# Performance work log

Measured on AMD Instinct MI355X. Metric: run time of the kernel, lower is better.

The kernel has to match this reference:

```python
import jax, jax.numpy as jnp
import numpy as np

LN_EPS = 1e-5

def setup_inputs() -> dict:
    key = jax.random.key(0)
    ks = jax.random.split(key, 8)
    B, N, C = 8, 16384, 256
    x = jax.random.normal(ks[0], (B, N, C), dtype=jnp.float32)
    time_decay = jax.random.normal(ks[1], (C,), dtype=jnp.float32) * 0.1
    s = 1.0 / np.sqrt(C)
    W_k = jax.random.normal(ks[2], (C, C), dtype=jnp.float32) * s
    W_v = jax.random.normal(ks[3], (C, C), dtype=jnp.float32) * s
    W_r = jax.random.normal(ks[4], (C, C), dtype=jnp.float32) * s
    W_o = jax.random.normal(ks[5], (C, C), dtype=jnp.float32) * s
    ln_w = jnp.ones((C,), dtype=jnp.float32)
    ln_b = jnp.zeros((C,), dtype=jnp.float32)
    return {"x": x, "time_decay": time_decay, "W_k": W_k, "W_v": W_v,
            "W_r": W_r, "W_o": W_o, "ln_w": ln_w, "ln_b": ln_b}

def _layernorm(x, w, b):
    mu = jnp.mean(x, axis=-1, keepdims=True)
    var = jnp.mean(jnp.square(x - mu), axis=-1, keepdims=True)
    return (x - mu) * jax.lax.rsqrt(var + LN_EPS) * w + b

def reference(x, time_decay, W_k, W_v, W_r, W_o, ln_w, ln_b):
    # x: (B, N, C)
    xn = _layernorm(x, ln_w, ln_b)
    k = jnp.einsum('bnc,dc->bnd', xn, W_k)
    v = jnp.einsum('bnc,dc->bnd', xn, W_v)
    r = jax.nn.sigmoid(jnp.einsum('bnc,dc->bnd', xn, W_r))
    decay = jnp.exp(-jax.nn.relu(time_decay))  # (C,)

    def step(state, k_t):
        state = state * decay + k_t  # (B, C)
        return state, state

    k_tm = jnp.swapaxes(k, 0, 1)  # (N, B, C) time-major for scan
    init = jnp.zeros(k.shape[::2], dtype=x.dtype)  # (B, C)
    _, states = jax.lax.scan(step, init, k_tm)
    states = jnp.swapaxes(states, 0, 1)  # (B, N, C)
    y = r * (states + v)
    y = jnp.einsum('bnc,dc->bnd', y, W_o)
    return y
```

## Files before the change

kernel.cpp:

```cpp
#include <hip/hip_runtime.h>
#include <hip/hip_bf16.h>
#include <stdint.h>


typedef __attribute__((ext_vector_type(8))) short short8;
typedef __attribute__((ext_vector_type(4))) float f32x4;

static __device__ __forceinline__ unsigned short f2bf(float f) {
  __hip_bfloat16 h = __float2bfloat16(f);
  return *reinterpret_cast<unsigned short*>(&h);
}
static __device__ __forceinline__ float bf2f(unsigned short u) {
  unsigned int v = ((unsigned int)u) << 16;
  float f;
  __builtin_memcpy(&f, &v, 4);
  return f;
}

__global__ void ln_kernel(const float* __restrict__ x,
                          const float* __restrict__ w,
                          const float* __restrict__ b,
                          unsigned short* __restrict__ xn) {
  const int wv = threadIdx.x >> 6;
  const int ln = threadIdx.x & 63;
  const size_t row = (size_t)blockIdx.x * 4 + wv;
  const float4 v = reinterpret_cast<const float4*>(x)[row * 64 + ln];
  float s  = v.x + v.y + v.z + v.w;
  float sq = v.x * v.x + v.y * v.y + v.z * v.z + v.w * v.w;
#pragma unroll
  for (int off = 32; off; off >>= 1) {
    s  += __shfl_xor(s, off, 64);
    sq += __shfl_xor(sq, off, 64);
  }
  const float mu  = s * (1.0f / 256.0f);
  const float var = sq * (1.0f / 256.0f) - mu * mu;
  const float rs  = rsqrtf(var + 1e-5f);
  const float4 w4 = reinterpret_cast<const float4*>(w)[ln];
  const float4 b4 = reinterpret_cast<const float4*>(b)[ln];
  ushort4 o;
  o.x = f2bf((v.x - mu) * rs * w4.x + b4.x);
  o.y = f2bf((v.y - mu) * rs * w4.y + b4.y);
  o.z = f2bf((v.z - mu) * rs * w4.z + b4.z);
  o.w = f2bf((v.w - mu) * rs * w4.w + b4.w);
  reinterpret_cast<ushort4*>(xn)[row * 64 + ln] = o;
}

__global__ void cvt_weights(const float* __restrict__ Wk,
                            const float* __restrict__ Wv,
                            const float* __restrict__ Wr,
                            const float* __restrict__ Wo,
                            unsigned short* __restrict__ Wkvr,
                            unsigned short* __restrict__ Wob) {
  const int idx = blockIdx.x * 256 + threadIdx.x;
  if (idx < 768 * 256) {
    const int r = idx >> 8;
    const int c = idx & 255;
    const float* src = (r < 256) ? Wk : ((r < 512) ? Wv : Wr);
    Wkvr[idx] = f2bf(src[(r & 255) * 256 + c]);
  } else {
    const int j = idx - 768 * 256;
    Wob[j] = f2bf(Wo[j]);
  }
}

template <int EPI, int NY>
__global__ void gemm_bt(const unsigned short* __restrict__ A,
                        const unsigned short* __restrict__ Bt,
                        unsigned short* __restrict__ kbuf,
                        unsigned short* __restrict__ vbuf,
                        unsigned short* __restrict__ rbuf,
                        float* __restrict__ outf) {
  constexpr int K = 256;
  __shared__ unsigned short Als[128][64];
  __shared__ unsigned short Bls[128][64];

  const int tid = threadIdx.x;
  const int wv = tid >> 6;
  const int ln = tid & 63;
  const int bid = blockIdx.x;
  const int bm0 = (bid / NY) * 128;
  const int bn0 = (bid % NY) * 128;
  const int lq = ln >> 4;
  const int lm = ln & 15;

  f32x4 acc[4][4];
#pragma unroll
  for (int i = 0; i < 4; ++i)
#pragma unroll
    for (int j = 0; j < 4; ++j) acc[i][j] = (f32x4){0.f, 0.f, 0.f, 0.f};

  const int m0w = (wv >> 1) * 64;
  const int n0w = (wv & 1) * 64;

  const int srow = ln >> 3;
  const int schunk = (ln & 7) ^ srow;

  for (int kk0 = 0; kk0 < K; kk0 += 64) {
#pragma unroll
    for (int i = 0; i < 4; ++i) {
      const int rr = wv * 32 + i * 8;
      const unsigned short* gA = A + (size_t)(bm0 + rr + srow) * K + kk0 + schunk * 8;
      __builtin_amdgcn_global_load_lds(
          (const __attribute__((address_space(1))) void*)gA,
          (__attribute__((address_space(3))) void*)&Als[rr][0], 16, 0, 0);
      const unsigned short* gB = Bt + (size_t)(bn0 + rr + srow) * K + kk0 + schunk * 8;
      __builtin_amdgcn_global_load_lds(
          (const __attribute__((address_space(1))) void*)gB,
          (__attribute__((address_space(3))) void*)&Bls[rr][0], 16, 0, 0);
    }
    __syncthreads();
#pragma unroll
    for (int kk = 0; kk < 64; kk += 32) {
      short8 af[4], bfr[4];
      const int chunk = (kk >> 3) + lq;
#pragma unroll
      for (int t = 0; t < 4; ++t) {
        const int rowa = m0w + t * 16 + lm;
        af[t] = *reinterpret_cast<const short8*>(&Als[rowa][(chunk ^ (rowa & 7)) * 8]);
        const int rowb = n0w + t * 16 + lm;
        bfr[t] = *reinterpret_cast<const short8*>(&Bls[rowb][(chunk ^ (rowb & 7)) * 8]);
      }
#pragma unroll
      for (int mt = 0; mt < 4; ++mt)
#pragma unroll
        for (int nt = 0; nt < 4; ++nt)
          acc[mt][nt] = __builtin_amdgcn_mfma_f32_16x16x32_bf16(
              bfr[nt], af[mt], acc[mt][nt], 0, 0, 0);
    }
    __syncthreads();
  }

#pragma unroll
  for (int mt = 0; mt < 4; ++mt) {
    const int m_g = bm0 + m0w + mt * 16 + lm;
#pragma unroll
    for (int nt = 0; nt < 4; ++nt) {
      const int n_base = bn0 + n0w + nt * 16 + lq * 4;
      f32x4 a = acc[mt][nt];
      if (EPI == 0) {
        const int bufi = n_base >> 8;
        const int col = n_base & 255;
        unsigned short* dst = (bufi == 0) ? kbuf : ((bufi == 1) ? vbuf : rbuf);
        if (bufi == 2) {
#pragma unroll
          for (int r = 0; r < 4; ++r) a[r] = 1.0f / (1.0f + __expf(-a[r]));
        }
        ushort4 pk;
        pk.x = f2bf(a[0]); pk.y = f2bf(a[1]); pk.z = f2bf(a[2]); pk.w = f2bf(a[3]);
        *reinterpret_cast<ushort4*>(&dst[(size_t)m_g * 256 + col]) = pk;
      } else {
        float4 o = make_float4(a[0], a[1], a[2], a[3]);
        *reinterpret_cast<float4*>(&outf[(size_t)m_g * 256 + n_base]) = o;
      }
    }
  }
}

__global__ void scan_carry(const unsigned short* __restrict__ k,
                           const float* __restrict__ td,
                           float* __restrict__ carry) {
  const int lane32 = threadIdx.x & 31;
  const int sub = threadIdx.x >> 5;
  const int bch = blockIdx.x * 8 + sub;
  const int c0 = lane32 * 8;
  float d[8], s[8];
#pragma unroll
  for (int j = 0; j < 8; ++j) {
    d[j] = expf(-fmaxf(td[c0 + j], 0.0f));
    s[j] = 0.0f;
  }
  const unsigned short* kp = k + (size_t)bch * 64 * 256 + c0;
#pragma unroll 4
  for (int i = 0; i < 64; ++i) {
    short8 kv = *reinterpret_cast<const short8*>(kp + (size_t)i * 256);
#pragma unroll
    for (int j = 0; j < 8; ++j) s[j] = s[j] * d[j] + bf2f((unsigned short)kv[j]);
  }
  float4* cp = reinterpret_cast<float4*>(carry + (size_t)bch * 256 + c0);
  cp[0] = make_float4(s[0], s[1], s[2], s[3]);
  cp[1] = make_float4(s[4], s[5], s[6], s[7]);
}

__global__ void scan_chunks(float* __restrict__ carry,
                            const float* __restrict__ td) {
  const int b = blockIdx.x;
  const int c = threadIdx.x;
  const float dL = expf(-fmaxf(td[c], 0.0f) * 64.0f);
  float s = 0.0f;
  float* base = carry + (size_t)b * 256 * 256 + c;
  for (int j0 = 0; j0 < 256; j0 += 8) {
    float buf[8];
#pragma unroll
    for (int t = 0; t < 8; ++t) buf[t] = base[(size_t)(j0 + t) * 256];
#pragma unroll
    for (int t = 0; t < 8; ++t) {
      base[(size_t)(j0 + t) * 256] = s;
      s = dL * s + buf[t];
    }
  }
}

__global__ void scan_final(unsigned short* __restrict__ k,
                           const unsigned short* __restrict__ v,
                           const unsigned short* __restrict__ r,
                           const float* __restrict__ carryin,
                           const float* __restrict__ td) {
  const int lane32 = threadIdx.x & 31;
  const int sub = threadIdx.x >> 5;
  const int bch = blockIdx.x * 8 + sub;
  const int c0 = lane32 * 8;
  float d[8], s[8];
  const float4* ci = reinterpret_cast<const float4*>(carryin + (size_t)bch * 256 + c0);
  float4 c0v = ci[0], c1v = ci[1];
  s[0] = c0v.x; s[1] = c0v.y; s[2] = c0v.z; s[3] = c0v.w;
  s[4] = c1v.x; s[5] = c1v.y; s[6] = c1v.z; s[7] = c1v.w;
#pragma unroll
  for (int j = 0; j < 8; ++j) d[j] = expf(-fmaxf(td[c0 + j], 0.0f));
  const size_t base = (size_t)bch * 64 * 256 + c0;
#pragma unroll 2
  for (int i = 0; i < 64; ++i) {
    const size_t off = base + (size_t)i * 256;
    short8 kv = *reinterpret_cast<const short8*>(k + off);
    short8 vv = *reinterpret_cast<const short8*>(v + off);
    short8 rv = *reinterpret_cast<const short8*>(r + off);
    short8 y;
#pragma unroll
    for (int j = 0; j < 8; ++j) {
      s[j] = s[j] * d[j] + bf2f((unsigned short)kv[j]);
      const float yj = bf2f((unsigned short)rv[j]) * (s[j] + bf2f((unsigned short)vv[j]));
      y[j] = (short)f2bf(yj);
    }
    *reinterpret_cast<short8*>(k + off) = y;
  }
}

extern "C" void kernel_launch(void* const* d_in, const int* in_sizes, int n_in,
                              void* d_out, int out_size, void* d_ws, size_t ws_size,
                              hipStream_t stream) {
  const float* x   = (const float*)d_in[0];
  const float* td  = (const float*)d_in[1];
  const float* Wk  = (const float*)d_in[2];
  const float* Wv  = (const float*)d_in[3];
  const float* Wr  = (const float*)d_in[4];
  const float* Wo  = (const float*)d_in[5];
  const float* lnw = (const float*)d_in[6];
  const float* lnb = (const float*)d_in[7];
  float* out = (float*)d_out;

  const int Bsz = 8, C = 256;
  const size_t M = 131072;

  char* ws = (char*)d_ws;
  size_t off = 0;
  auto alloc = [&](size_t bytes) -> char* {
    char* p = ws + off;
    off += (bytes + 255) & ~(size_t)255;
    return p;
  };
  unsigned short* xn   = (unsigned short*)alloc(M * C * 2);
  unsigned short* kbuf = (unsigned short*)alloc(M * C * 2);
  unsigned short* vbuf = (unsigned short*)alloc(M * C * 2);
  unsigned short* rbuf = (unsigned short*)alloc(M * C * 2);
  unsigned short* Wkvr = (unsigned short*)alloc(768 * 256 * 2);
  unsigned short* Wob  = (unsigned short*)alloc(256 * 256 * 2);
  float* carry = (float*)alloc((size_t)Bsz * 256 * C * 4);
  (void)ws_size; (void)in_sizes; (void)n_in; (void)out_size;

  cvt_weights<<<dim3(1024), dim3(256), 0, stream>>>(Wk, Wv, Wr, Wo, Wkvr, Wob);
  ln_kernel<<<dim3((unsigned)(M / 4)), dim3(256), 0, stream>>>(x, lnw, lnb, xn);
  gemm_bt<0, 6><<<dim3(1024 * 6), dim3(256), 0, stream>>>(
      xn, Wkvr, kbuf, vbuf, rbuf, nullptr);
  scan_carry<<<dim3(256), dim3(256), 0, stream>>>(kbuf, td, carry);
  scan_chunks<<<dim3(Bsz), dim3(256), 0, stream>>>(carry, td);
  scan_final<<<dim3(256), dim3(256), 0, stream>>>(kbuf, vbuf, rbuf, carry, td);
  gemm_bt<1, 2><<<dim3(1024 * 2), dim3(256), 0, stream>>>(
      kbuf, Wob, nullptr, nullptr, nullptr, out);
}
```

Measured before the change: 440.3 us.

## Fuse chunk carry computation into KVR GEMM epilogue and remap blocks per XCD

```diff
diff --git a/kernel.cpp b/kernel.cpp
--- a/kernel.cpp
+++ b/kernel.cpp
@@ -69,7 +69,9 @@
                         unsigned short* __restrict__ kbuf,
                         unsigned short* __restrict__ vbuf,
                         unsigned short* __restrict__ rbuf,
-                        float* __restrict__ outf) {
+                        float* __restrict__ outf,
+                        const float* __restrict__ td,
+                        float* __restrict__ carry) {
   constexpr int K = 256;
   __shared__ unsigned short Als[128][64];
   __shared__ unsigned short Bls[128][64];
@@ -77,7 +79,9 @@
   const int tid = threadIdx.x;
   const int wv = tid >> 6;
   const int ln = tid & 63;
-  const int bid = blockIdx.x;
+  const int cpx = (int)gridDim.x >> 3;
+  const int hw = (int)blockIdx.x;
+  const int bid = (hw & 7) * cpx + (hw >> 3);
   const int bm0 = (bid / NY) * 128;
   const int bn0 = (bid % NY) * 128;
   const int lq = ln >> 4;
@@ -154,31 +158,36 @@
       }
     }
   }
-}
-
-__global__ void scan_carry(const unsigned short* __restrict__ k,
-                           const float* __restrict__ td,
-                           float* __restrict__ carry) {
-  const int lane32 = threadIdx.x & 31;
-  const int sub = threadIdx.x >> 5;
-  const int bch = blockIdx.x * 8 + sub;
-  const int c0 = lane32 * 8;
-  float d[8], s[8];
-#pragma unroll
-  for (int j = 0; j < 8; ++j) {
-    d[j] = expf(-fmaxf(td[c0 + j], 0.0f));
-    s[j] = 0.0f;
-  }
-  const unsigned short* kp = k + (size_t)bch * 64 * 256 + c0;
-#pragma unroll 4
-  for (int i = 0; i < 64; ++i) {
-    short8 kv = *reinterpret_cast<const short8*>(kp + (size_t)i * 256);
-#pragma unroll
-    for (int j = 0; j < 8; ++j) s[j] = s[j] * d[j] + bf2f((unsigned short)kv[j]);
-  }
-  float4* cp = reinterpret_cast<float4*>(carry + (size_t)bch * 256 + c0);
-  cp[0] = make_float4(s[0], s[1], s[2], s[3]);
-  cp[1] = make_float4(s[4], s[5], s[6], s[7]);
+
+  if (EPI == 0 && bn0 < 256) {
+    const int chk = (bm0 + m0w) >> 6;
+#pragma unroll
+    for (int nt = 0; nt < 4; ++nt) {
+      const int cb = bn0 + n0w + nt * 16 + lq * 4;
+      const float4 td4 = *reinterpret_cast<const float4*>(&td[cb]);
+      float sum[4];
+      const float tdv[4] = {td4.x, td4.y, td4.z, td4.w};
+#pragma unroll
+      for (int r = 0; r < 4; ++r) {
+        const float t = fmaxf(tdv[r], 0.0f);
+        const float g = expf(16.0f * t);
+        float h = acc[3][nt][r];
+        h = h * g + acc[2][nt][r];
+        h = h * g + acc[1][nt][r];
+        h = h * g + acc[0][nt][r];
+        sum[r] = h * expf(-t * (float)(63 - lm));
+      }
+#pragma unroll
+      for (int off = 1; off < 16; off <<= 1) {
+#pragma unroll
+        for (int r = 0; r < 4; ++r) sum[r] += __shfl_xor(sum[r], off, 64);
+      }
+      if (lm == 0) {
+        *reinterpret_cast<float4*>(&carry[(size_t)chk * 256 + cb]) =
+            make_float4(sum[0], sum[1], sum[2], sum[3]);
+      }
+    }
+  }
 }
 
 __global__ void scan_chunks(float* __restrict__ carry,
@@ -269,10 +278,9 @@
   cvt_weights<<<dim3(1024), dim3(256), 0, stream>>>(Wk, Wv, Wr, Wo, Wkvr, Wob);
   ln_kernel<<<dim3((unsigned)(M / 4)), dim3(256), 0, stream>>>(x, lnw, lnb, xn);
   gemm_bt<0, 6><<<dim3(1024 * 6), dim3(256), 0, stream>>>(
-      xn, Wkvr, kbuf, vbuf, rbuf, nullptr);
-  scan_carry<<<dim3(256), dim3(256), 0, stream>>>(kbuf, td, carry);
+      xn, Wkvr, kbuf, vbuf, rbuf, nullptr, td, carry);
   scan_chunks<<<dim3(Bsz), dim3(256), 0, stream>>>(carry, td);
   scan_final<<<dim3(256), dim3(256), 0, stream>>>(kbuf, vbuf, rbuf, carry, td);
   gemm_bt<1, 2><<<dim3(1024 * 2), dim3(256), 0, stream>>>(
-      kbuf, Wob, nullptr, nullptr, nullptr, out);
-}
+      kbuf, Wob, nullptr, nullptr, nullptr, out, nullptr, nullptr);
+}
```

Result: no change. 448.6 us (+1.9%).

## Widen GEMM tiles to 128x256 with 8 waves and XCD-aware block remap

Applied to the files above, without the earlier changes.

```diff
diff --git a/kernel.cpp b/kernel.cpp
--- a/kernel.cpp
+++ b/kernel.cpp
@@ -64,22 +64,25 @@
 }
 
 template <int EPI, int NY>
-__global__ void gemm_bt(const unsigned short* __restrict__ A,
-                        const unsigned short* __restrict__ Bt,
-                        unsigned short* __restrict__ kbuf,
-                        unsigned short* __restrict__ vbuf,
-                        unsigned short* __restrict__ rbuf,
-                        float* __restrict__ outf) {
+__global__ __launch_bounds__(512, 4) void gemm_bt(
+    const unsigned short* __restrict__ A,
+    const unsigned short* __restrict__ Bt,
+    unsigned short* __restrict__ kbuf,
+    unsigned short* __restrict__ vbuf,
+    unsigned short* __restrict__ rbuf,
+    float* __restrict__ outf) {
   constexpr int K = 256;
   __shared__ unsigned short Als[128][64];
-  __shared__ unsigned short Bls[128][64];
+  __shared__ unsigned short Bls[256][64];
 
   const int tid = threadIdx.x;
   const int wv = tid >> 6;
   const int ln = tid & 63;
-  const int bid = blockIdx.x;
+  const int cpx = (int)gridDim.x >> 3;
+  const int hw = (int)blockIdx.x;
+  const int bid = (hw & 7) * cpx + (hw >> 3);
   const int bm0 = (bid / NY) * 128;
-  const int bn0 = (bid % NY) * 128;
+  const int bn0 = (bid % NY) * 256;
   const int lq = ln >> 4;
   const int lm = ln & 15;
 
@@ -89,36 +92,50 @@
 #pragma unroll
     for (int j = 0; j < 4; ++j) acc[i][j] = (f32x4){0.f, 0.f, 0.f, 0.f};
 
-  const int m0w = (wv >> 1) * 64;
-  const int n0w = (wv & 1) * 64;
+  const int m0w = (wv >> 2) * 64;
+  const int n0w = (wv & 3) * 64;
 
   const int srow = ln >> 3;
   const int schunk = (ln & 7) ^ srow;
 
+  const int ra = wv * 16;
+  const int rb = wv * 32;
+
   for (int kk0 = 0; kk0 < K; kk0 += 64) {
-#pragma unroll
-    for (int i = 0; i < 4; ++i) {
-      const int rr = wv * 32 + i * 8;
-      const unsigned short* gA = A + (size_t)(bm0 + rr + srow) * K + kk0 + schunk * 8;
+    {
+      const unsigned short* gA =
+          A + (size_t)(bm0 + ra + srow) * K + kk0 + schunk * 8;
       __builtin_amdgcn_global_load_lds(
           (const __attribute__((address_space(1))) void*)gA,
-          (__attribute__((address_space(3))) void*)&Als[rr][0], 16, 0, 0);
-      const unsigned short* gB = Bt + (size_t)(bn0 + rr + srow) * K + kk0 + schunk * 8;
+          (__attribute__((address_space(3))) void*)&Als[ra][0], 16, 0, 0);
+      __builtin_amdgcn_global_load_lds(
+          (const __attribute__((address_space(1))) void*)(gA + 8 * K),
+          (__attribute__((address_space(3))) void*)&Als[ra + 8][0], 16, 0, 0);
+      const unsigned short* gB =
+          Bt + (size_t)(bn0 + rb + srow) * K + kk0 + schunk * 8;
       __builtin_amdgcn_global_load_lds(
           (const __attribute__((address_space(1))) void*)gB,
-          (__attribute__((address_space(3))) void*)&Bls[rr][0], 16, 0, 0);
+          (__attribute__((address_space(3))) void*)&Bls[rb][0], 16, 0, 0);
+      __builtin_amdgcn_global_load_lds(
+          (const __attribute__((address_space(1))) void*)(gB + 8 * K),
+          (__attribute__((address_space(3))) void*)&Bls[rb + 8][0], 16, 0, 0);
+      __builtin_amdgcn_global_load_lds(
+          (const __attribute__((address_space(1))) void*)(gB + 16 * K),
+          (__attribute__((address_space(3))) void*)&Bls[rb + 16][0], 16, 0, 0);
+      __builtin_amdgcn_global_load_lds(
+          (const __attribute__((address_space(1))) void*)(gB + 24 * K),
+          (__attribute__((address_space(3))) void*)&Bls[rb + 24][0], 16, 0, 0);
     }
     __syncthreads();
 #pragma unroll
     for (int kk = 0; kk < 64; kk += 32) {
       short8 af[4], bfr[4];
       const int chunk = (kk >> 3) + lq;
+      const int sw = chunk ^ (lm & 7);
 #pragma unroll
       for (int t = 0; t < 4; ++t) {
-        const int rowa = m0w + t * 16 + lm;
-        af[t] = *reinterpret_cast<const short8*>(&Als[rowa][(chunk ^ (rowa & 7)) * 8]);
-        const int rowb = n0w + t * 16 + lm;
-        bfr[t] = *reinterpret_cast<const short8*>(&Bls[rowb][(chunk ^ (rowb & 7)) * 8]);
+        af[t] = *reinterpret_cast<const short8*>(&Als[m0w + t * 16 + lm][sw * 8]);
+        bfr[t] = *reinterpret_cast<const short8*>(&Bls[n0w + t * 16 + lm][sw * 8]);
       }
 #pragma unroll
       for (int mt = 0; mt < 4; ++mt)
@@ -135,11 +152,10 @@
     const int m_g = bm0 + m0w + mt * 16 + lm;
 #pragma unroll
     for (int nt = 0; nt < 4; ++nt) {
-      const int n_base = bn0 + n0w + nt * 16 + lq * 4;
+      const int col = n0w + nt * 16 + lq * 4;
       f32x4 a = acc[mt][nt];
       if (EPI == 0) {
-        const int bufi = n_base >> 8;
-        const int col = n_base & 255;
+        const int bufi = bn0 >> 8;
         unsigned short* dst = (bufi == 0) ? kbuf : ((bufi == 1) ? vbuf : rbuf);
         if (bufi == 2) {
 #pragma unroll
@@ -150,7 +166,7 @@
         *reinterpret_cast<ushort4*>(&dst[(size_t)m_g * 256 + col]) = pk;
       } else {
         float4 o = make_float4(a[0], a[1], a[2], a[3]);
-        *reinterpret_cast<float4*>(&outf[(size_t)m_g * 256 + n_base]) = o;
+        *reinterpret_cast<float4*>(&outf[(size_t)m_g * 256 + col]) = o;
       }
     }
   }
@@ -268,11 +284,11 @@
 
   cvt_weights<<<dim3(1024), dim3(256), 0, stream>>>(Wk, Wv, Wr, Wo, Wkvr, Wob);
   ln_kernel<<<dim3((unsigned)(M / 4)), dim3(256), 0, stream>>>(x, lnw, lnb, xn);
-  gemm_bt<0, 6><<<dim3(1024 * 6), dim3(256), 0, stream>>>(
+  gemm_bt<0, 3><<<dim3(3072), dim3(512), 0, stream>>>(
       xn, Wkvr, kbuf, vbuf, rbuf, nullptr);
   scan_carry<<<dim3(256), dim3(256), 0, stream>>>(kbuf, td, carry);
   scan_chunks<<<dim3(Bsz), dim3(256), 0, stream>>>(carry, td);
   scan_final<<<dim3(256), dim3(256), 0, stream>>>(kbuf, vbuf, rbuf, carry, td);
-  gemm_bt<1, 2><<<dim3(1024 * 2), dim3(256), 0, stream>>>(
+  gemm_bt<1, 1><<<dim3(1024), dim3(512), 0, stream>>>(
       kbuf, Wob, nullptr, nullptr, nullptr, out);
 }
```

Result: no change. 446.5 us (+1.4%).
